# Optimization experiments

Hardware: AMD Instinct MI355X
Metric: run time of the kernel (lower is better)

Reference implementation:

```python
import jax, jax.numpy as jnp
import numpy as np

OUT = 50000   # out_features = connectivity rows
IN = 50000    # in_features  = connectivity cols
NNZ = 1_600_000  # avg degree 32
B = 512       # batch (leading dims of x)


def setup_inputs() -> dict:
    key = jax.random.key(0)
    k1, k2, k3, k4 = jax.random.split(key, 4)
    x = jax.random.normal(k1, (B, IN), dtype=jnp.float32)
    rows = jax.random.randint(k2, (NNZ,), 0, OUT, dtype=jnp.int32)
    cols = jax.random.randint(k3, (NNZ,), 0, IN, dtype=jnp.int32)
    indices = jnp.stack([rows, cols])            # [2, NNZ] COO indices
    values = jax.random.normal(k4, (NNZ,), dtype=jnp.float32)
    bias = jnp.zeros((OUT, 1), dtype=jnp.float32)  # module initializes bias to zeros
    return {"x": x, "indices": indices, "values": values, "bias": bias}


def reference(x, indices, values, bias):
    # feature_dim=-1: permute features to dim 0 -> x_t is (IN, B)
    row, col = indices[0], indices[1]
    x_t = x.T                                    # (IN, B)
    # spmm: for each nnz, values[e] * x_t[col[e]] accumulated into row[e]
    contrib = values[:, None] * x_t[col]         # (NNZ, B)
    y = jax.ops.segment_sum(contrib, row, num_segments=OUT)  # (OUT, B)
    y = y + bias                                 # bias is (OUT, 1), broadcasts
    return y.T                                   # permute back -> (B, OUT)
```

## Files before the change

kernel.cpp:

```cpp
#include <hip/hip_runtime.h>
#include <hip/hip_bf16.h>


typedef float f32x4 __attribute__((ext_vector_type(4)));

#define CT_SHIFT 11

__global__ __launch_bounds__(256) void transpose_bf16_v2(
        const float* __restrict__ in,
        __hip_bfloat16* __restrict__ out,
        int rows, int cols) {
    __shared__ __hip_bfloat16 T[64][72];
    const int t  = threadIdx.x;
    const int c0 = blockIdx.x * 64;
    const int r0 = blockIdx.y * 64;

    {
        const int tx = t & 15, ty = t >> 4;
        const int c = c0 + tx * 4;
        for (int p = 0; p < 4; ++p) {
            const int rl = ty + p * 16;
            const int r = r0 + rl;
            float fx = 0.f, fy = 0.f, fz = 0.f, fw = 0.f;
            if (r < rows && c + 3 < cols) {
                f32x4 f = __builtin_nontemporal_load(
                    (const f32x4*)(in + (size_t)r * cols + c));
                fx = f.x; fy = f.y; fz = f.z; fw = f.w;
            } else if (r < rows) {
                const float* p0 = in + (size_t)r * cols;
                if (c + 0 < cols) fx = p0[c + 0];
                if (c + 1 < cols) fy = p0[c + 1];
                if (c + 2 < cols) fz = p0[c + 2];
                if (c + 3 < cols) fw = p0[c + 3];
            }
            T[tx * 4 + 0][rl] = __float2bfloat16(fx);
            T[tx * 4 + 1][rl] = __float2bfloat16(fy);
            T[tx * 4 + 2][rl] = __float2bfloat16(fz);
            T[tx * 4 + 3][rl] = __float2bfloat16(fw);
        }
    }
    __syncthreads();
    {
        const int cl0 = t >> 3;
        const int rq  = t & 7;
        const int rl  = rq * 8;
        const int r   = r0 + rl;
        for (int q = 0; q < 2; ++q) {
            const int cl = q * 32 + cl0;
            const int c  = c0 + cl;
            if (c < cols) {
                if (r + 7 < rows) {
                    *(uint4*)(out + (size_t)c * rows + r) =
                        *(const uint4*)&T[cl][rl];
                } else {
                    for (int j = 0; j < 8 && r + j < rows; ++j)
                        out[(size_t)c * rows + r + j] = T[cl][rl + j];
                }
            }
        }
    }
}

__global__ __launch_bounds__(256) void transpose32_v2(
        const float* __restrict__ in,
        float* __restrict__ out,
        int rows, int cols) {
    __shared__ float T[64][68];
    const int t  = threadIdx.x;
    const int c0 = blockIdx.x * 64;
    const int r0 = blockIdx.y * 64;

    {
        const int tx = t & 15, ty = t >> 4;
        const int c = c0 + tx * 4;
        for (int p = 0; p < 4; ++p) {
            const int rl = ty + p * 16;
            const int r = r0 + rl;
            float fx = 0.f, fy = 0.f, fz = 0.f, fw = 0.f;
            if (r < rows && c + 3 < cols) {
                const float4 f = *(const float4*)(in + (size_t)r * cols + c);
                fx = f.x; fy = f.y; fz = f.z; fw = f.w;
            } else if (r < rows) {
                const float* p0 = in + (size_t)r * cols;
                if (c + 0 < cols) fx = p0[c + 0];
                if (c + 1 < cols) fy = p0[c + 1];
                if (c + 2 < cols) fz = p0[c + 2];
                if (c + 3 < cols) fw = p0[c + 3];
            }
            T[tx * 4 + 0][rl] = fx;
            T[tx * 4 + 1][rl] = fy;
            T[tx * 4 + 2][rl] = fz;
            T[tx * 4 + 3][rl] = fw;
        }
    }
    __syncthreads();
    {
        const int rq  = t & 15;
        const int cl0 = t >> 4;
        const int rl  = rq * 4;
        const int r   = r0 + rl;
        for (int p = 0; p < 4; ++p) {
            const int cl = p * 16 + cl0;
            const int c  = c0 + cl;
            if (c < cols) {
                if (r + 3 < rows) {
                    f32x4 f;
                    f.x = T[cl][rl + 0]; f.y = T[cl][rl + 1];
                    f.z = T[cl][rl + 2]; f.w = T[cl][rl + 3];
                    __builtin_nontemporal_store(
                        f, (f32x4*)(out + (size_t)c * rows + r));
                } else {
                    for (int j = 0; j < 4 && r + j < rows; ++j)
                        out[(size_t)c * rows + r + j] = T[cl][rl + j];
                }
            }
        }
    }
}

__global__ void zero_i32_kernel(int* __restrict__ p, int n) {
    int i = blockIdx.x * blockDim.x + threadIdx.x;
    if (i < n) p[i] = 0;
}

__global__ void hist_kernel(const int* __restrict__ rows,
                            const int* __restrict__ cols, int nnz,
                            int* __restrict__ counts, int NT) {
    int e = blockIdx.x * blockDim.x + threadIdx.x;
    if (e < nnz) {
        int r = __builtin_nontemporal_load(rows + e);
        int c = __builtin_nontemporal_load(cols + e);
        atomicAdd(&counts[r * NT + (c >> CT_SHIFT)], 1);
    }
}

#define SCAN_T 256
#define SCAN_CHUNK 2048
#define MAX_CHUNKS 1024

__global__ __launch_bounds__(SCAN_T) void scan1_kernel(
        const int* __restrict__ counts, int* __restrict__ offsets,
        int* __restrict__ bsum, int n) {
    __shared__ int sdata[SCAN_T];
    int t = threadIdx.x;
    int base_i = blockIdx.x * SCAN_CHUNK + t * 8;
    int vals[8];
    int tot = 0;
#pragma unroll
    for (int j = 0; j < 8; ++j) {
        int i = base_i + j;
        int v = (i < n) ? counts[i] : 0;
        tot += v;
        vals[j] = tot;
    }
    sdata[t] = tot;
    __syncthreads();
    for (int off = 1; off < SCAN_T; off <<= 1) {
        int x = (t >= off) ? sdata[t - off] : 0;
        __syncthreads();
        sdata[t] += x;
        __syncthreads();
    }
    int tbase = (t > 0) ? sdata[t - 1] : 0;
#pragma unroll
    for (int j = 0; j < 8; ++j) {
        int i = base_i + j;
        if (i < n) offsets[i + 1] = tbase + vals[j];
    }
    if (t == SCAN_T - 1) bsum[blockIdx.x] = sdata[SCAN_T - 1];
}

__global__ void scan2_kernel(int* __restrict__ bsum, int nb) {
    if (threadIdx.x == 0 && blockIdx.x == 0) {
        int run = 0;
        for (int i = 0; i < nb; ++i) { int v = bsum[i]; bsum[i] = run; run += v; }
    }
}

__global__ void scan3_kernel(int* __restrict__ offsets,
                             const int* __restrict__ bsum, int n) {
    int i = blockIdx.x * blockDim.x + threadIdx.x;
    if (i == 0) offsets[0] = 0;
    if (i < n) offsets[i + 1] += bsum[i / SCAN_CHUNK];
}

__global__ void scatter_kernel(const int* __restrict__ rows,
                               const int* __restrict__ cols,
                               const float* __restrict__ vals, int nnz,
                               const int* __restrict__ offsets,
                               int* __restrict__ counts,
                               int2* __restrict__ edges, int NT) {
    int e = blockIdx.x * blockDim.x + threadIdx.x;
    if (e < nnz) {
        int r = __builtin_nontemporal_load(rows + e);
        int c = __builtin_nontemporal_load(cols + e);
        float v = __builtin_nontemporal_load(vals + e);
        int k = r * NT + (c >> CT_SHIFT);
        int p = offsets[k] + atomicSub(&counts[k], 1) - 1;
        edges[p] = make_int2(c, __float_as_int(v));
    }
}

__device__ __forceinline__ float bf_lo(unsigned u) {
    return __uint_as_float(u << 16);
}
__device__ __forceinline__ float bf_hi(unsigned u) {
    return __uint_as_float(u & 0xffff0000u);
}

__global__ __launch_bounds__(256) void spmm_kernel(
        const ushort* __restrict__ xT,
        const int* __restrict__ offsets,
        const int2* __restrict__ edges,
        const float* __restrict__ bias,
        float* __restrict__ y,
        int B, int OUTn, int NT) {
    const int lane = threadIdx.x & 63;
    const int r = blockIdx.x * 4 + (threadIdx.x >> 6);
    if (r >= OUTn) return;
    const int e0 = offsets[(size_t)r * NT];
    const int e1 = offsets[(size_t)(r + 1) * NT];
    const float bv = bias[r];
    const ushort* xb = xT + (size_t)(lane << 3);

    float a0 = 0.f, a1 = 0.f, a2 = 0.f, a3 = 0.f;
    float a4 = 0.f, a5 = 0.f, a6 = 0.f, a7 = 0.f;

    int e = e0;
    for (; e + 2 <= e1; e += 2) {
        const int2 d0 = edges[e];
        const int2 d1 = edges[e + 1];
        const uint4 u0 = *(const uint4*)(xb + (size_t)d0.x * B);
        const uint4 u1 = *(const uint4*)(xb + (size_t)d1.x * B);
        const float v0 = __int_as_float(d0.y);
        const float v1 = __int_as_float(d1.y);
        a0 += v0 * bf_lo(u0.x); a1 += v0 * bf_hi(u0.x);
        a2 += v0 * bf_lo(u0.y); a3 += v0 * bf_hi(u0.y);
        a4 += v0 * bf_lo(u0.z); a5 += v0 * bf_hi(u0.z);
        a6 += v0 * bf_lo(u0.w); a7 += v0 * bf_hi(u0.w);
        a0 += v1 * bf_lo(u1.x); a1 += v1 * bf_hi(u1.x);
        a2 += v1 * bf_lo(u1.y); a3 += v1 * bf_hi(u1.y);
        a4 += v1 * bf_lo(u1.z); a5 += v1 * bf_hi(u1.z);
        a6 += v1 * bf_lo(u1.w); a7 += v1 * bf_hi(u1.w);
    }
    if (e < e1) {
        const int2 d0 = edges[e];
        const uint4 u0 = *(const uint4*)(xb + (size_t)d0.x * B);
        const float v0 = __int_as_float(d0.y);
        a0 += v0 * bf_lo(u0.x); a1 += v0 * bf_hi(u0.x);
        a2 += v0 * bf_lo(u0.y); a3 += v0 * bf_hi(u0.y);
        a4 += v0 * bf_lo(u0.z); a5 += v0 * bf_hi(u0.z);
        a6 += v0 * bf_lo(u0.w); a7 += v0 * bf_hi(u0.w);
    }

    float* yp = y + (size_t)r * B + (size_t)(lane << 3);
    *(float4*)(yp)     = make_float4(a0 + bv, a1 + bv, a2 + bv, a3 + bv);
    *(float4*)(yp + 4) = make_float4(a4 + bv, a5 + bv, a6 + bv, a7 + bv);
}

extern "C" void kernel_launch(void* const* d_in, const int* in_sizes, int n_in,
                              void* d_out, int out_size, void* d_ws, size_t ws_size,
                              hipStream_t stream) {
    const float* x       = (const float*)d_in[0];
    const int*   indices = (const int*)  d_in[1];
    const float* values  = (const float*)d_in[2];
    const float* bias    = (const float*)d_in[3];

    float* out = (float*)d_out;

    const int NNZ = in_sizes[2];
    const int OUT = in_sizes[3];
    const int B   = out_size / OUT;
    const int IN  = (int)((size_t)in_sizes[0] / (size_t)B);

    const int* rows = indices;
    const int* cols = indices + NNZ;

    const int NT   = (IN + (1 << CT_SHIFT) - 1) >> CT_SHIFT;
    const int NKEY = OUT * NT;

    char* ws = (char*)d_ws;
    __hip_bfloat16* xT = (__hip_bfloat16*)ws;  ws += (size_t)IN * B * sizeof(__hip_bfloat16);
    float* y       = (float*)ws;  ws += (size_t)OUT * B * sizeof(float);
    int2*  edges   = (int2*)ws;   ws += (size_t)NNZ * sizeof(int2);
    int*   counts  = (int*)ws;    ws += (size_t)NKEY * sizeof(int);
    int*   offsets = (int*)ws;    ws += ((size_t)NKEY + 4) * sizeof(int);
    int*   bsum    = (int*)ws;    ws += MAX_CHUNKS * sizeof(int);

    const int nchunks = (NKEY + SCAN_CHUNK - 1) / SCAN_CHUNK;

    transpose_bf16_v2<<<dim3((IN + 63) / 64, (B + 63) / 64), 256, 0, stream>>>(
        x, xT, B, IN);

    zero_i32_kernel<<<(NKEY + 255) / 256, 256, 0, stream>>>(counts, NKEY);
    hist_kernel<<<(NNZ + 255) / 256, 256, 0, stream>>>(rows, cols, NNZ, counts, NT);
    scan1_kernel<<<nchunks, SCAN_T, 0, stream>>>(counts, offsets, bsum, NKEY);
    scan2_kernel<<<1, 64, 0, stream>>>(bsum, nchunks);
    scan3_kernel<<<(NKEY + 255) / 256, 256, 0, stream>>>(offsets, bsum, NKEY);
    scatter_kernel<<<(NNZ + 255) / 256, 256, 0, stream>>>(
        rows, cols, values, NNZ, offsets, counts, edges, NT);

    spmm_kernel<<<(OUT + 3) / 4, 256, 0, stream>>>(
        (const ushort*)xT, offsets, edges, bias, y, B, OUT, NT);

    transpose32_v2<<<dim3((B + 63) / 64, (OUT + 63) / 64), 256, 0, stream>>>(
        y, out, OUT, B);
}
```

Before: 649.7 us.

## Fuse output transpose into SpMM via shared memory and parallelize block-sum scan

```diff
diff --git a/kernel.cpp b/kernel.cpp
--- a/kernel.cpp
+++ b/kernel.cpp
@@ -69,7 +69,6 @@
     const int t  = threadIdx.x;
     const int c0 = blockIdx.x * 64;
     const int r0 = blockIdx.y * 64;
-
     {
         const int tx = t & 15, ty = t >> 4;
         const int c = c0 + tx * 4;
@@ -170,10 +169,33 @@
     if (t == SCAN_T - 1) bsum[blockIdx.x] = sdata[SCAN_T - 1];
 }
 
-__global__ void scan2_kernel(int* __restrict__ bsum, int nb) {
-    if (threadIdx.x == 0 && blockIdx.x == 0) {
-        int run = 0;
-        for (int i = 0; i < nb; ++i) { int v = bsum[i]; bsum[i] = run; run += v; }
+__global__ __launch_bounds__(256) void scan2_kernel(int* __restrict__ bsum,
+                                                    int nb) {
+    __shared__ int sdata[256];
+    const int t = threadIdx.x;
+    const int base = t * 4;
+    int vals[4];
+    int tot = 0;
+#pragma unroll
+    for (int j = 0; j < 4; ++j) {
+        int i = base + j;
+        int x = (i < nb) ? bsum[i] : 0;
+        vals[j] = tot;
+        tot += x;
+    }
+    sdata[t] = tot;
+    __syncthreads();
+    for (int off = 1; off < 256; off <<= 1) {
+        int x = (t >= off) ? sdata[t - off] : 0;
+        __syncthreads();
+        sdata[t] += x;
+        __syncthreads();
+    }
+    const int tbase = (t > 0) ? sdata[t - 1] : 0;
+#pragma unroll
+    for (int j = 0; j < 4; ++j) {
+        int i = base + j;
+        if (i < nb) bsum[i] = tbase + vals[j];
     }
 }
 
@@ -208,24 +230,11 @@
     return __uint_as_float(u & 0xffff0000u);
 }
 
-__global__ __launch_bounds__(256) void spmm_kernel(
-        const ushort* __restrict__ xT,
-        const int* __restrict__ offsets,
-        const int2* __restrict__ edges,
-        const float* __restrict__ bias,
-        float* __restrict__ y,
-        int B, int OUTn, int NT) {
-    const int lane = threadIdx.x & 63;
-    const int r = blockIdx.x * 4 + (threadIdx.x >> 6);
-    if (r >= OUTn) return;
-    const int e0 = offsets[(size_t)r * NT];
-    const int e1 = offsets[(size_t)(r + 1) * NT];
-    const float bv = bias[r];
-    const ushort* xb = xT + (size_t)(lane << 3);
-
-    float a0 = 0.f, a1 = 0.f, a2 = 0.f, a3 = 0.f;
-    float a4 = 0.f, a5 = 0.f, a6 = 0.f, a7 = 0.f;
-
+__device__ __forceinline__ void row_accum(
+        const ushort* __restrict__ xb, const int2* __restrict__ edges,
+        int e0, int e1, int B,
+        float& a0, float& a1, float& a2, float& a3,
+        float& a4, float& a5, float& a6, float& a7) {
     int e = e0;
     for (; e + 2 <= e1; e += 2) {
         const int2 d0 = edges[e];
@@ -252,6 +261,74 @@
         a4 += v0 * bf_lo(u0.z); a5 += v0 * bf_hi(u0.z);
         a6 += v0 * bf_lo(u0.w); a7 += v0 * bf_hi(u0.w);
     }
+}
+
+__global__ __launch_bounds__(1024) void spmm_fused_kernel(
+        const ushort* __restrict__ xT,
+        const int* __restrict__ offsets,
+        const int2* __restrict__ edges,
+        const float* __restrict__ bias,
+        float* __restrict__ outp,
+        int OUTn, int NT) {
+    __shared__ float Ty[16][516];
+    const int w    = threadIdx.x >> 6;
+    const int lane = threadIdx.x & 63;
+    const int r    = blockIdx.x * 16 + w;
+    const int B    = 512;
+
+    float a0 = 0.f, a1 = 0.f, a2 = 0.f, a3 = 0.f;
+    float a4 = 0.f, a5 = 0.f, a6 = 0.f, a7 = 0.f;
+    {
+        const int e0 = offsets[(size_t)r * NT];
+        const int e1 = offsets[(size_t)(r + 1) * NT];
+        const float bv = bias[r];
+        const ushort* xb = xT + (size_t)(lane << 3);
+        row_accum(xb, edges, e0, e1, B, a0, a1, a2, a3, a4, a5, a6, a7);
+        a0 += bv; a1 += bv; a2 += bv; a3 += bv;
+        a4 += bv; a5 += bv; a6 += bv; a7 += bv;
+    }
+
+    {
+        float* p = &Ty[w][lane << 3];
+        f32x4 f0, f1;
+        f0.x = a0; f0.y = a1; f0.z = a2; f0.w = a3;
+        f1.x = a4; f1.y = a5; f1.z = a6; f1.w = a7;
+        *(f32x4*)(p)     = f0;
+        *(f32x4*)(p + 4) = f1;
+    }
+    __syncthreads();
+    {
+        const int b  = threadIdx.x & 511;
+        const int rq = (threadIdx.x >> 9) << 3;
+        f32x4 f0, f1;
+        f0.x = Ty[rq + 0][b]; f0.y = Ty[rq + 1][b];
+        f0.z = Ty[rq + 2][b]; f0.w = Ty[rq + 3][b];
+        f1.x = Ty[rq + 4][b]; f1.y = Ty[rq + 5][b];
+        f1.z = Ty[rq + 6][b]; f1.w = Ty[rq + 7][b];
+        float* op = outp + (size_t)b * OUTn + blockIdx.x * 16 + rq;
+        *(f32x4*)(op)     = f0;
+        *(f32x4*)(op + 4) = f1;
+    }
+}
+
+__global__ __launch_bounds__(256) void spmm_kernel(
+        const ushort* __restrict__ xT,
+        const int* __restrict__ offsets,
+        const int2* __restrict__ edges,
+        const float* __restrict__ bias,
+        float* __restrict__ y,
+        int B, int OUTn, int NT) {
+    const int lane = threadIdx.x & 63;
+    const int r = blockIdx.x * 4 + (threadIdx.x >> 6);
+    if (r >= OUTn) return;
+    const int e0 = offsets[(size_t)r * NT];
+    const int e1 = offsets[(size_t)(r + 1) * NT];
+    const float bv = bias[r];
+    const ushort* xb = xT + (size_t)(lane << 3);
+
+    float a0 = 0.f, a1 = 0.f, a2 = 0.f, a3 = 0.f;
+    float a4 = 0.f, a5 = 0.f, a6 = 0.f, a7 = 0.f;
+    row_accum(xb, edges, e0, e1, B, a0, a1, a2, a3, a4, a5, a6, a7);
 
     float* yp = y + (size_t)r * B + (size_t)(lane << 3);
     *(float4*)(yp)     = make_float4(a0 + bv, a1 + bv, a2 + bv, a3 + bv);
@@ -295,14 +372,18 @@
     zero_i32_kernel<<<(NKEY + 255) / 256, 256, 0, stream>>>(counts, NKEY);
     hist_kernel<<<(NNZ + 255) / 256, 256, 0, stream>>>(rows, cols, NNZ, counts, NT);
     scan1_kernel<<<nchunks, SCAN_T, 0, stream>>>(counts, offsets, bsum, NKEY);
-    scan2_kernel<<<1, 64, 0, stream>>>(bsum, nchunks);
+    scan2_kernel<<<1, 256, 0, stream>>>(bsum, nchunks);
     scan3_kernel<<<(NKEY + 255) / 256, 256, 0, stream>>>(offsets, bsum, NKEY);
     scatter_kernel<<<(NNZ + 255) / 256, 256, 0, stream>>>(
         rows, cols, values, NNZ, offsets, counts, edges, NT);
 
-    spmm_kernel<<<(OUT + 3) / 4, 256, 0, stream>>>(
-        (const ushort*)xT, offsets, edges, bias, y, B, OUT, NT);
-
-    transpose32_v2<<<dim3((B + 63) / 64, (OUT + 63) / 64), 256, 0, stream>>>(
-        y, out, OUT, B);
-}
+    if (B == 512 && (OUT & 15) == 0) {
+        spmm_fused_kernel<<<OUT / 16, 1024, 0, stream>>>(
+            (const ushort*)xT, offsets, edges, bias, out, OUT, NT);
+    } else {
+        spmm_kernel<<<(OUT + 3) / 4, 256, 0, stream>>>(
+            (const ushort*)xT, offsets, edges, bias, y, B, OUT, NT);
+        transpose32_v2<<<dim3((B + 63) / 64, (OUT + 63) / 64), 256, 0, stream>>>(
+            y, out, OUT, B);
+    }
+}
```

After: 579.2 us. -10.9%, faster.
